# Optimization experiments

Measured on AMD Instinct MI355X. Metric: run time of the kernel, lower is better.

## Reference

```python
import jax, jax.numpy as jnp
import numpy as np

# Model/config dims (Llama-3-8B style attention, GQA 32q/8kv)
B, S, HID = 4, 512, 4096
NH, NKV, D = 32, 8, 128
CAP = 2048          # KV cache capacity
MAXPOS = 2048       # max_position_embeddings
START = 1024        # kvcache_start_index (uniform across batch -> static masking)
EPS = 1e-6
QK_SCALE = 1.0 / float(D) ** 0.5
NEG = -1e9


def setup_inputs() -> dict:
    key = jax.random.key(0)
    ks = jax.random.split(key, 8)
    w = 0.02  # weight init scale
    return {
        'hidden_states': jax.random.normal(ks[0], (B, S, HID), jnp.float32),
        'k_cache': jax.random.normal(ks[1], (B, NKV, CAP, D), jnp.float32),
        'v_cache': jax.random.normal(ks[2], (B, NKV, CAP, D), jnp.float32),
        'rope_rotary_cos_sin': jax.random.uniform(ks[3], (B, MAXPOS, D), jnp.float32),
        'context_lengths': jnp.full((B,), S, jnp.int32),
        'kvcache_start_index': jnp.full((B,), START, jnp.int32),
        'Wq': jax.random.normal(ks[4], (HID, NH * D), jnp.float32) * w,
        'Wk': jax.random.normal(ks[5], (HID, NKV * D), jnp.float32) * w,
        'Wv': jax.random.normal(ks[6], (HID, NKV * D), jnp.float32) * w,
        'Wo': jax.random.normal(ks[7], (NH * D, HID), jnp.float32) * w,
        'q_norm_w': jnp.ones((D,), jnp.float32),
        'k_norm_w': jnp.ones((D,), jnp.float32),
    }


def _rmsnorm(x, w):
    # per-head RMSNorm over head_dim (Qwen3-style QK norm)
    return x * jax.lax.rsqrt(jnp.mean(x * x, axis=-1, keepdims=True) + EPS) * w


def _apply_rope(x, cos, sin, pos):
    # x: [B,H,S,D]; cos/sin: [MAXPOS, D/2]; pos: [B,S]
    c = cos[pos][:, None, :, :]  # [B,1,S,D/2]
    s = sin[pos][:, None, :, :]
    x1, x2 = jnp.split(x, 2, axis=-1)
    return jnp.concatenate([x1 * c - x2 * s, x2 * c + x1 * s], axis=-1)


def reference(hidden_states, k_cache, v_cache, rope_rotary_cos_sin,
              context_lengths, kvcache_start_index,
              Wq, Wk, Wv, Wo, q_norm_w, k_norm_w):
    b, s, _ = hidden_states.shape
    # fused QKV projection
    q = (hidden_states @ Wq).reshape(b, s, NH, D)
    k = (hidden_states @ Wk).reshape(b, s, NKV, D)
    v = (hidden_states @ Wv).reshape(b, s, NKV, D)
    # QK norm
    q = _rmsnorm(q, q_norm_w)
    k = _rmsnorm(k, k_norm_w)
    # [B,H,S,D]
    q = q.transpose(0, 2, 1, 3)
    k = k.transpose(0, 2, 1, 3)
    v = v.transpose(0, 2, 1, 3)
    # RoPE tables: first half cos, second half sin; batch dim 0 only
    half = D // 2
    cos = rope_rotary_cos_sin[0, :, :half]
    sin = rope_rotary_cos_sin[0, :, half:]
    pos = kvcache_start_index[:, None] + jnp.arange(s, dtype=kvcache_start_index.dtype)[None, :]
    q = _apply_rope(q, cos, sin, pos)
    k = _apply_rope(k, cos, sin, pos)
    # KV cache update: write new k/v at per-batch start index
    def upd(cache, new, st):  # cache [H,CAP,D], new [H,S,D]
        return jax.lax.dynamic_update_slice(cache, new, (0, st, 0))
    present_k = jax.vmap(upd)(k_cache, k, kvcache_start_index)
    present_v = jax.vmap(upd)(v_cache, v, kvcache_start_index)
    # GQA: expand kv heads to attention heads
    g = NH // NKV
    kf = jnp.repeat(present_k, g, axis=1)  # [B,NH,CAP,D]
    vf = jnp.repeat(present_v, g, axis=1)
    # scaled attention over cache; mask cols beyond absolute query position
    scores = jnp.einsum('bhsd,bhtd->bhst', q * QK_SCALE, kf)
    col = jnp.arange(CAP, dtype=pos.dtype)
    allowed = col[None, None, :] <= pos[:, :, None]        # [B,S,CAP]
    scores = jnp.where(allowed[:, None, :, :], scores, NEG)
    attn = jax.nn.softmax(scores, axis=-1)
    out = jnp.einsum('bhst,bhtd->bhsd', attn, vf)
    out = out.transpose(0, 2, 1, 3).reshape(b, s, NH * D)
    out = out @ Wo
    return out, present_k, present_v
```

## Files before the change

### kernel.cpp

```cpp
#include <hip/hip_runtime.h>
#include <hip/hip_bf16.h>
#include <cstdint>

#define Bsz   4
#define Ssz   512
#define HIDsz 4096
#define NHsz  32
#define NKVsz 8
#define Dsz   128
#define CAPsz 2048
#define EPSf  1e-6f
#define QK_SCALEf 0.08838834764831845f

typedef __attribute__((ext_vector_type(8))) short short8;
typedef __attribute__((ext_vector_type(4))) float f32x4;

__device__ __forceinline__ unsigned short f2bf(float x) {
    unsigned u = __float_as_uint(x);
    return (unsigned short)((u + 0x7fffu + ((u >> 16) & 1u)) >> 16);
}

__device__ __forceinline__ void gload16(const void* g, void* l) {
    __builtin_amdgcn_global_load_lds(
        (const __attribute__((address_space(1))) unsigned int*)g,
        (__attribute__((address_space(3))) unsigned int*)l, 16, 0, 0);
}

__global__ __launch_bounds__(256) void convert_bf16_kernel(
    const float* __restrict__ in, unsigned short* __restrict__ out, int n4)
{
    int i = blockIdx.x * blockDim.x + threadIdx.x;
    if (i < n4) {
        float4 v = ((const float4*)in)[i];
        ushort4 o;
        o.x = f2bf(v.x); o.y = f2bf(v.y); o.z = f2bf(v.z); o.w = f2bf(v.w);
        ((ushort4*)out)[i] = o;
    }
}

__global__ __launch_bounds__(256) void transpose_bf16_kernel(
    const float* __restrict__ W, unsigned short* __restrict__ Wt, int K, int N)
{
    __shared__ float tile[64][65];
    const int k0 = blockIdx.y * 64, n0 = blockIdx.x * 64;
    const int t = threadIdx.x;
    const int tr = t >> 4, tc4 = (t & 15) * 4;
#pragma unroll
    for (int i = 0; i < 4; i++) {
        int r = tr + i * 16;
        float4 v = *(const float4*)(W + (size_t)(k0 + r) * N + n0 + tc4);
        tile[r][tc4 + 0] = v.x; tile[r][tc4 + 1] = v.y;
        tile[r][tc4 + 2] = v.z; tile[r][tc4 + 3] = v.w;
    }
    __syncthreads();
#pragma unroll
    for (int i = 0; i < 4; i++) {
        int nr = tr + i * 16;
        ushort4 o;
        o.x = f2bf(tile[tc4 + 0][nr]);
        o.y = f2bf(tile[tc4 + 1][nr]);
        o.z = f2bf(tile[tc4 + 2][nr]);
        o.w = f2bf(tile[tc4 + 3][nr]);
        *(ushort4*)(Wt + (size_t)(n0 + nr) * K + k0 + tc4) = o;
    }
}

__global__ __launch_bounds__(256) void transpose_v_kernel(
    const float* __restrict__ V, unsigned short* __restrict__ Vt)
{
    __shared__ float tile[64][65];
    const int c0 = blockIdx.x * 64, d0 = blockIdx.y * 64, bk = blockIdx.z;
    const int t = threadIdx.x;
    const int tr = t >> 4, tc4 = (t & 15) * 4;
    const float* base = V + (size_t)bk * CAPsz * Dsz;
#pragma unroll
    for (int i = 0; i < 4; i++) {
        int r = tr + i * 16;
        float4 v = *(const float4*)(base + (size_t)(c0 + r) * Dsz + d0 + tc4);
        tile[r][tc4 + 0] = v.x; tile[r][tc4 + 1] = v.y;
        tile[r][tc4 + 2] = v.z; tile[r][tc4 + 3] = v.w;
    }
    __syncthreads();
    unsigned short* ob = Vt + (size_t)bk * Dsz * CAPsz;
#pragma unroll
    for (int i = 0; i < 4; i++) {
        int dr = tr + i * 16;
        ushort4 o;
        o.x = f2bf(tile[tc4 + 0][dr]);
        o.y = f2bf(tile[tc4 + 1][dr]);
        o.z = f2bf(tile[tc4 + 2][dr]);
        o.w = f2bf(tile[tc4 + 3][dr]);
        *(ushort4*)(ob + (size_t)(d0 + dr) * CAPsz + c0 + tc4) = o;
    }
}

template<int MODE>
__global__ __launch_bounds__(256, 2) void gemm_bf16_kernel(
    const unsigned short* __restrict__ A,
    const unsigned short* __restrict__ Bt,
    float* __restrict__ C, int M, int N, int K,
    const int* __restrict__ start_idx)
{
    __shared__ __align__(16) unsigned short As[128 * 64];
    __shared__ __align__(16) unsigned short Bs[128 * 64];
    const int t    = threadIdx.x;
    const int lane = t & 63, wv = t >> 6;
    const int m0 = blockIdx.y * 128, n0 = blockIdx.x * 128;
    const int rw = (wv & 1) * 64, cw = (wv >> 1) * 64;

    f32x4 acc[4][4];
#pragma unroll
    for (int r = 0; r < 4; r++)
#pragma unroll
        for (int c = 0; c < 4; c++) acc[r][c] = (f32x4){0.f, 0.f, 0.f, 0.f};

    const int arow = lane >> 3;
    const int acol = (lane & 7) * 8;
    const int fr = lane & 15, fq = (lane >> 4) * 8;

    for (int k0 = 0; k0 < K; k0 += 64) {
        __syncthreads();
#pragma unroll
        for (int i = 0; i < 4; i++) {
            int ro = (i * 4 + wv) * 8;
            gload16(A  + (size_t)(m0 + ro + arow) * K + k0 + acol, As + (size_t)ro * 64);
            gload16(Bt + (size_t)(n0 + ro + arow) * K + k0 + acol, Bs + (size_t)ro * 64);
        }
        __syncthreads();
#pragma unroll
        for (int kk = 0; kk < 2; kk++) {
            short8 af[4], bfr[4];
#pragma unroll
            for (int r = 0; r < 4; r++)
                af[r] = *(const short8*)&As[(rw + r * 16 + fr) * 64 + kk * 32 + fq];
#pragma unroll
            for (int c = 0; c < 4; c++)
                bfr[c] = *(const short8*)&Bs[(cw + c * 16 + fr) * 64 + kk * 32 + fq];
#pragma unroll
            for (int r = 0; r < 4; r++)
#pragma unroll
                for (int c = 0; c < 4; c++)
                    acc[r][c] = __builtin_amdgcn_mfma_f32_16x16x32_bf16(
                        af[r], bfr[c], acc[r][c], 0, 0, 0);
        }
    }

    int pos0 = 0;
    if (MODE == 1) pos0 = start_idx[m0 >> 9];
#pragma unroll
    for (int r = 0; r < 4; r++) {
#pragma unroll
        for (int c = 0; c < 4; c++) {
            int col = n0 + cw + c * 16 + (lane & 15);
#pragma unroll
            for (int reg = 0; reg < 4; reg++) {
                int row = m0 + rw + r * 16 + (lane >> 4) * 4 + reg;
                float val = acc[r][c][reg];
                if (MODE == 0) {
                    C[(size_t)row * N + col] = val;
                } else {
                    int pos = pos0 + (row & (Ssz - 1));
                    int kvh = col >> 7, d = col & 127;
                    int b = row >> 9;
                    C[((size_t)(b * NKVsz + kvh) * CAPsz + pos) * Dsz + d] = val;
                }
            }
        }
    }
}

__global__ __launch_bounds__(256) void rmsnorm_rope_kernel(
    float* __restrict__ X, unsigned short* __restrict__ Xbf,
    const float* __restrict__ w,
    const float* __restrict__ rope, const int* __restrict__ start_idx,
    int nheads, int mode)
{
    int gid   = blockIdx.x * blockDim.x + threadIdx.x;
    int wid   = gid >> 6;
    int lane  = threadIdx.x & 63;
    int token = wid / nheads;
    int h     = wid - token * nheads;
    int b = token >> 9, s = token & (Ssz - 1);
    int pos = start_idx[b] + s;
    float* row;
    if (mode == 0) row = X + (size_t)token * (nheads * Dsz) + h * Dsz;
    else           row = X + ((size_t)(b * nheads + h) * CAPsz + pos) * Dsz;

    float x1 = row[lane], x2 = row[lane + 64];
    float ss = x1 * x1 + x2 * x2;
#pragma unroll
    for (int off = 32; off > 0; off >>= 1) ss += __shfl_xor(ss, off);
    float rn  = rsqrtf(ss * (1.f / 128.f) + EPSf);
    float xn1 = x1 * rn * w[lane];
    float xn2 = x2 * rn * w[lane + 64];
    float c   = rope[(size_t)pos * Dsz + lane];
    float sn  = rope[(size_t)pos * Dsz + 64 + lane];
    float o1 = xn1 * c - xn2 * sn;
    float o2 = xn2 * c + xn1 * sn;
    if (mode == 0) {
        unsigned short* orow = Xbf + (size_t)token * (nheads * Dsz) + h * Dsz;
        orow[lane]      = f2bf(o1 * QK_SCALEf);
        orow[lane + 64] = f2bf(o2 * QK_SCALEf);
    } else {
        row[lane]      = o1;
        row[lane + 64] = o2;
    }
}

__global__ __launch_bounds__(256, 2) void attn_mfma_kernel(
    const unsigned short* __restrict__ Qbf,
    const unsigned short* __restrict__ Kbf,
    const unsigned short* __restrict__ Vtbf,
    unsigned short* __restrict__ O,
    const int* __restrict__ start_idx)
{
    __shared__ __align__(16) unsigned short Ks[64 * 128];
    __shared__ __align__(16) unsigned short Vs[128 * 64];
    __shared__ __align__(16) unsigned short Ps[4][32 * 72];

    const int t = threadIdx.x, lane = t & 63, wv = t >> 6;
    const int l15 = lane & 15, l4 = lane >> 4;
    const int qt = blockIdx.x, kv = blockIdx.y, b = blockIdx.z;
    const int h = kv * 4 + wv;
    const int s0 = qt * 32;
    const int start = start_idx[b];

    const int swz = (l15 & 7) << 3;

    short8 aq[2][4];
    const unsigned short* qb = Qbf + ((size_t)(b * Ssz + s0)) * HIDsz + h * Dsz;
#pragma unroll
    for (int m2 = 0; m2 < 2; m2++)
#pragma unroll
        for (int kq = 0; kq < 4; kq++)
            aq[m2][kq] = *(const short8*)(qb + (size_t)(m2 * 16 + l15) * HIDsz + kq * 32 + l4 * 8);

    f32x4 Oacc[2][8];
    float m_run[2][4], l_run[2][4];
#pragma unroll
    for (int m2 = 0; m2 < 2; m2++) {
#pragma unroll
        for (int nd = 0; nd < 8; nd++) Oacc[m2][nd] = (f32x4){0.f, 0.f, 0.f, 0.f};
#pragma unroll
        for (int r = 0; r < 4; r++) { m_run[m2][r] = -1e30f; l_run[m2][r] = 0.f; }
    }

    const unsigned short* kb = Kbf + (size_t)(b * NKVsz + kv) * CAPsz * Dsz;
    const unsigned short* vb = Vtbf + (size_t)(b * NKVsz + kv) * (size_t)Dsz * CAPsz;

    int t_hi = start + s0 + 31;
    if (t_hi > CAPsz - 1) t_hi = CAPsz - 1;

    for (int t0 = 0; t0 <= t_hi; t0 += 64) {
        __syncthreads();
#pragma unroll
        for (int i = 0; i < 4; i++) {
            int ro = (i * 4 + wv) * 4;
            int krow = ro + l4;
            gload16(kb + (size_t)(t0 + krow) * Dsz + ((l15 * 8) ^ ((krow & 7) << 3)),
                    Ks + ro * 128);
        }
#pragma unroll
        for (int i = 0; i < 4; i++) {
            int ro = (i * 4 + wv) * 8;
            int vrow = ro + (lane >> 3);
            gload16(vb + (size_t)vrow * CAPsz + t0 + (((lane & 7) * 8) ^ ((vrow & 7) << 3)),
                    Vs + ro * 64);
        }
        __syncthreads();

        f32x4 Sacc[2][4];
#pragma unroll
        for (int m2 = 0; m2 < 2; m2++)
#pragma unroll
            for (int n = 0; n < 4; n++) Sacc[m2][n] = (f32x4){0.f, 0.f, 0.f, 0.f};
#pragma unroll
        for (int kq = 0; kq < 4; kq++) {
            short8 bk[4];
#pragma unroll
            for (int n = 0; n < 4; n++)
                bk[n] = *(const short8*)&Ks[(n * 16 + l15) * 128 + ((kq * 32 + l4 * 8) ^ swz)];
#pragma unroll
            for (int m2 = 0; m2 < 2; m2++)
#pragma unroll
                for (int n = 0; n < 4; n++)
                    Sacc[m2][n] = __builtin_amdgcn_mfma_f32_16x16x32_bf16(
                        aq[m2][kq], bk[n], Sacc[m2][n], 0, 0, 0);
        }

        bool need_mask = (t0 + 63) > (start + s0);
#pragma unroll
        for (int m2 = 0; m2 < 2; m2++) {
#pragma unroll
            for (int reg = 0; reg < 4; reg++) {
                int rloc = m2 * 16 + l4 * 4 + reg;
                int row_pos = start + s0 + rloc;
                float sv[4];
#pragma unroll
                for (int n = 0; n < 4; n++) {
                    sv[n] = Sacc[m2][n][reg];
                    if (need_mask && (t0 + n * 16 + l15 > row_pos)) sv[n] = -1e30f;
                }
                float mrow = fmaxf(fmaxf(sv[0], sv[1]), fmaxf(sv[2], sv[3]));
#pragma unroll
                for (int off = 1; off < 16; off <<= 1)
                    mrow = fmaxf(mrow, __shfl_xor(mrow, off));
                float m_new = fmaxf(m_run[m2][reg], mrow);
                float alpha = __expf(m_run[m2][reg] - m_new);
                float ps = 0.f;
#pragma unroll
                for (int n = 0; n < 4; n++) {
                    sv[n] = __expf(sv[n] - m_new);
                    ps += sv[n];
                }
#pragma unroll
                for (int off = 1; off < 16; off <<= 1)
                    ps += __shfl_xor(ps, off);
                l_run[m2][reg] = l_run[m2][reg] * alpha + ps;
                m_run[m2][reg] = m_new;
#pragma unroll
                for (int nd = 0; nd < 8; nd++) Oacc[m2][nd][reg] *= alpha;
#pragma unroll
                for (int n = 0; n < 4; n++)
                    Ps[wv][rloc * 72 + n * 16 + l15] = f2bf(sv[n]);
            }
        }

#pragma unroll
        for (int kp = 0; kp < 2; kp++) {
            short8 ap[2];
#pragma unroll
            for (int m2 = 0; m2 < 2; m2++)
                ap[m2] = *(const short8*)&Ps[wv][(m2 * 16 + l15) * 72 + kp * 32 + l4 * 8];
#pragma unroll
            for (int nd = 0; nd < 8; nd++) {
                short8 bv = *(const short8*)&Vs[(nd * 16 + l15) * 64 + ((kp * 32 + l4 * 8) ^ swz)];
#pragma unroll
                for (int m2 = 0; m2 < 2; m2++)
                    Oacc[m2][nd] = __builtin_amdgcn_mfma_f32_16x16x32_bf16(
                        ap[m2], bv, Oacc[m2][nd], 0, 0, 0);
            }
        }
    }

    unsigned short* ob = O + ((size_t)(b * Ssz + s0)) * HIDsz + h * Dsz;
#pragma unroll
    for (int m2 = 0; m2 < 2; m2++)
#pragma unroll
        for (int reg = 0; reg < 4; reg++) {
            int rloc = m2 * 16 + l4 * 4 + reg;
            float inv = 1.f / l_run[m2][reg];
#pragma unroll
            for (int nd = 0; nd < 8; nd++)
                ob[(size_t)rloc * HIDsz + nd * 16 + l15] = f2bf(Oacc[m2][nd][reg] * inv);
        }
}

extern "C" void kernel_launch(void* const* d_in, const int* in_sizes, int n_in,
                              void* d_out, int out_size, void* d_ws, size_t ws_size,
                              hipStream_t stream) {
    (void)in_sizes; (void)n_in; (void)out_size; (void)ws_size;
    const float* hidden    = (const float*)d_in[0];
    const float* k_cache   = (const float*)d_in[1];
    const float* v_cache   = (const float*)d_in[2];
    const float* rope      = (const float*)d_in[3];
    const int*   start_idx = (const int*)d_in[5];
    const float* Wq        = (const float*)d_in[6];
    const float* Wk        = (const float*)d_in[7];
    const float* Wv        = (const float*)d_in[8];
    const float* Wo        = (const float*)d_in[9];
    const float* q_norm_w  = (const float*)d_in[10];
    const float* k_norm_w  = (const float*)d_in[11];

    float* out   = (float*)d_out;
    float* out_k = out + (size_t)Bsz * Ssz * HIDsz;
    float* out_v = out_k + (size_t)Bsz * NKVsz * CAPsz * Dsz;

    char* ws = (char*)d_ws;
    float*          q_ws      = (float*)ws;
    unsigned short* Kbf       = (unsigned short*)ws;
    unsigned short* Vtbf      = (unsigned short*)(ws + (((size_t) 16) << 20));
    unsigned short* hidden_bf = (unsigned short*)(ws + (((size_t) 32) << 20));
    unsigned short* attn_bf   = (unsigned short*)(ws + (((size_t) 48) << 20));
    unsigned short* qbf       = (unsigned short*)(ws + (((size_t) 64) << 20));
    unsigned short* Wqo_t     = (unsigned short*)(ws + (((size_t) 80) << 20));
    unsigned short* Wk_t      = (unsigned short*)(ws + (((size_t)112) << 20));
    unsigned short* Wv_t      = (unsigned short*)(ws + (((size_t)120) << 20));

    const size_t cache_bytes = (size_t)Bsz * NKVsz * CAPsz * Dsz * sizeof(float);
    (void)hipMemcpyAsync(out_k, k_cache, cache_bytes, hipMemcpyDeviceToDevice, stream);
    (void)hipMemcpyAsync(out_v, v_cache, cache_bytes, hipMemcpyDeviceToDevice, stream);

    convert_bf16_kernel<<<8192, 256, 0, stream>>>(hidden, hidden_bf, 2048 * 4096 / 4);
    transpose_bf16_kernel<<<dim3(64, 64), 256, 0, stream>>>(Wq, Wqo_t, HIDsz, NHsz * Dsz);
    transpose_bf16_kernel<<<dim3(16, 64), 256, 0, stream>>>(Wk, Wk_t, HIDsz, NKVsz * Dsz);
    transpose_bf16_kernel<<<dim3(16, 64), 256, 0, stream>>>(Wv, Wv_t, HIDsz, NKVsz * Dsz);

    gemm_bf16_kernel<0><<<dim3(32, 16), 256, 0, stream>>>(hidden_bf, Wqo_t, q_ws, 2048, 4096, 4096, nullptr);
    gemm_bf16_kernel<1><<<dim3(8, 16), 256, 0, stream>>>(hidden_bf, Wk_t, out_k, 2048, 1024, 4096, start_idx);
    gemm_bf16_kernel<1><<<dim3(8, 16), 256, 0, stream>>>(hidden_bf, Wv_t, out_v, 2048, 1024, 4096, start_idx);

    rmsnorm_rope_kernel<<<16384, 256, 0, stream>>>(q_ws, qbf, q_norm_w, rope, start_idx, NHsz, 0);
    rmsnorm_rope_kernel<<<4096, 256, 0, stream>>>(out_k, nullptr, k_norm_w, rope, start_idx, NKVsz, 1);

    convert_bf16_kernel<<<8192, 256, 0, stream>>>(out_k, Kbf, Bsz * NKVsz * CAPsz * Dsz / 4);
    transpose_v_kernel<<<dim3(32, 2, 32), 256, 0, stream>>>(out_v, Vtbf);

    attn_mfma_kernel<<<dim3(16, NKVsz, Bsz), 256, 0, stream>>>(qbf, Kbf, Vtbf, attn_bf, start_idx);

    transpose_bf16_kernel<<<dim3(64, 64), 256, 0, stream>>>(Wo, Wqo_t, NHsz * Dsz, HIDsz);
    gemm_bf16_kernel<0><<<dim3(32, 16), 256, 0, stream>>>(attn_bf, Wqo_t, out, 2048, 4096, 4096, nullptr);
}
```

Baseline: 815.0 us.

## Register-prefetch next K/V tile during attention compute and raise MFMA wave priority

Replaces the direct global-to-LDS loads of each K/V tile with a register-staged software pipeline. The next tile is loaded into registers while the current tile is computed, then written to swizzled LDS after a barrier. The aim is to hide global memory latency behind the QK^T, softmax and PV work. It also raises wave priority around the MFMA blocks via s_setprio, at the cost of extra VGPRs for the staging registers, which may reduce occupancy.

```diff
diff --git a/kernel.cpp b/kernel.cpp
--- a/kernel.cpp
+++ b/kernel.cpp
@@ -251,29 +251,55 @@
     int t_hi = start + s0 + 31;
     if (t_hi > CAPsz - 1) t_hi = CAPsz - 1;
 
+    int krow[4], vrow[4];
+    unsigned short* kw[4];
+    unsigned short* vw[4];
+#pragma unroll
+    for (int i = 0; i < 4; i++) {
+        int kr = (i * 4 + wv) * 4 + l4;
+        krow[i] = kr;
+        kw[i] = &Ks[kr * 128 + ((l15 * 8) ^ ((kr & 7) << 3))];
+        int vr = (i * 4 + wv) * 8 + (lane >> 3);
+        vrow[i] = vr;
+        vw[i] = &Vs[vr * 64 + (((lane & 7) * 8) ^ ((vr & 7) << 3))];
+    }
+
+    short8 kreg[4], vreg[4];
+#pragma unroll
+    for (int i = 0; i < 4; i++) {
+        kreg[i] = *(const short8*)(kb + (size_t)krow[i] * Dsz + l15 * 8);
+        vreg[i] = *(const short8*)(vb + (size_t)vrow[i] * CAPsz + (lane & 7) * 8);
+    }
+
     for (int t0 = 0; t0 <= t_hi; t0 += 64) {
-        __syncthreads();
-#pragma unroll
-        for (int i = 0; i < 4; i++) {
-            int ro = (i * 4 + wv) * 4;
-            int krow = ro + l4;
-            gload16(kb + (size_t)(t0 + krow) * Dsz + ((l15 * 8) ^ ((krow & 7) << 3)),
-                    Ks + ro * 128);
-        }
-#pragma unroll
-        for (int i = 0; i < 4; i++) {
-            int ro = (i * 4 + wv) * 8;
-            int vrow = ro + (lane >> 3);
-            gload16(vb + (size_t)vrow * CAPsz + t0 + (((lane & 7) * 8) ^ ((vrow & 7) << 3)),
-                    Vs + ro * 64);
-        }
-        __syncthreads();
+        asm volatile("s_waitcnt lgkmcnt(0)" ::: "memory");
+        __builtin_amdgcn_s_barrier();
+        __builtin_amdgcn_sched_barrier(0);
+
+#pragma unroll
+        for (int i = 0; i < 4; i++) *(short8*)kw[i] = kreg[i];
+#pragma unroll
+        for (int i = 0; i < 4; i++) *(short8*)vw[i] = vreg[i];
+
+        if (t0 + 64 <= t_hi) {
+            int tn = t0 + 64;
+#pragma unroll
+            for (int i = 0; i < 4; i++) {
+                kreg[i] = *(const short8*)(kb + (size_t)(tn + krow[i]) * Dsz + l15 * 8);
+                vreg[i] = *(const short8*)(vb + (size_t)vrow[i] * CAPsz + tn + (lane & 7) * 8);
+            }
+        }
+
+        asm volatile("s_waitcnt lgkmcnt(0)" ::: "memory");
+        __builtin_amdgcn_s_barrier();
+        __builtin_amdgcn_sched_barrier(0);
 
         f32x4 Sacc[2][4];
 #pragma unroll
         for (int m2 = 0; m2 < 2; m2++)
 #pragma unroll
             for (int n = 0; n < 4; n++) Sacc[m2][n] = (f32x4){0.f, 0.f, 0.f, 0.f};
+        __builtin_amdgcn_s_setprio(1);
 #pragma unroll
         for (int kq = 0; kq < 4; kq++) {
             short8 bk[4];
@@ -287,6 +313,7 @@
                     Sacc[m2][n] = __builtin_amdgcn_mfma_f32_16x16x32_bf16(
                         aq[m2][kq], bk[n], Sacc[m2][n], 0, 0, 0);
         }
+        __builtin_amdgcn_s_setprio(0);
 
         bool need_mask = (t0 + 63) > (start + s0);
 #pragma unroll
@@ -326,6 +353,7 @@
             }
         }
 
+        __builtin_amdgcn_s_setprio(1);
 #pragma unroll
         for (int kp = 0; kp < 2; kp++) {
             short8 ap[2];
@@ -341,6 +369,7 @@
                         ap[m2], bv, Oacc[m2][nd], 0, 0, 0);
             }
         }
+        __builtin_amdgcn_s_setprio(0);
     }
 
     unsigned short* ob = O + ((size_t)(b * Ssz + s0)) * HIDsz + h * Dsz;
```

After: 806.7 us. About the same (-1.0%).
